# Performance work log

Measured on AMD Instinct MI355X. Metric: run time of the kernel, lower is better.

## Reference

```python
import jax, jax.numpy as jnp
import numpy as np

THRESHOLD = 0.05
TOP_N = 300
NMS_THR = 0.6
POST_TOP_N = 100
MIN_SIZE = 0
N_CLASS = 81
C = N_CLASS - 1
STRIDES = (8, 16, 32, 64, 128)
IMG_H, IMG_W = 800, 1024
B = 16


def _level_hw(s):
    return (-(-IMG_H // s), -(-IMG_W // s))


def setup_inputs() -> dict:
    key = jax.random.key(0)
    inp = {}
    for li, s in enumerate(STRIDES):
        H, W = _level_hw(s)
        key, k1, k2, k3 = jax.random.split(key, 4)
        xs = (jnp.arange(W, dtype=jnp.float32) + 0.5) * s
        ys = (jnp.arange(H, dtype=jnp.float32) + 0.5) * s
        gx, gy = jnp.meshgrid(xs, ys)  # [H, W], row-major h*W+w flatten order
        inp[f"location{li}"] = jnp.stack([gx.reshape(-1), gy.reshape(-1)], -1)
        inp[f"cls{li}"] = jax.random.normal(k1, (B, C, H, W), jnp.float32)
        inp[f"box{li}"] = jax.random.uniform(k2, (B, 4, H, W), jnp.float32) * (4.0 * s)
        inp[f"ctr{li}"] = jax.random.normal(k3, (B, 1, H, W), jnp.float32)
    inp["img_h"] = IMG_H
    inp["img_w"] = IMG_W
    return inp


def _process_level(loc, cls, box, ctr, img_h, img_w):
    b, c, h, w = cls.shape
    cls = jax.nn.sigmoid(cls.transpose(0, 2, 3, 1).reshape(b, h * w, c))
    box = box.transpose(0, 2, 3, 1).reshape(b, h * w, 4)
    ctr = jax.nn.sigmoid(ctr.reshape(b, h * w))
    score = cls * ctr[:, :, None]                 # [B, HW, C]
    masked = jnp.where(cls > THRESHOLD, score, -1.0).reshape(b, -1)
    k = min(TOP_N, masked.shape[1])
    vals, idx = jax.lax.top_k(masked, k)
    if k < TOP_N:
        vals = jnp.pad(vals, ((0, 0), (0, TOP_N - k)), constant_values=-1.0)
        idx = jnp.pad(idx, ((0, 0), (0, TOP_N - k)))
    valid = vals > 0.0                            # candidates only; pads invalid
    pos = idx // c
    label = idx % c + 1
    ssel = jnp.take_along_axis(score.reshape(b, -1), idx, axis=1)  # differentiable gather
    bsel = jnp.take_along_axis(box, pos[..., None], axis=1)        # [B, TOP_N, 4]
    lsel = loc[pos]                                                # [B, TOP_N, 2]
    # decode + clip (BoxList.clip clamps to [0, size-1])
    x1 = jnp.clip(lsel[..., 0] - bsel[..., 0], 0.0, img_w - 1.0)
    y1 = jnp.clip(lsel[..., 1] - bsel[..., 1], 0.0, img_h - 1.0)
    x2 = jnp.clip(lsel[..., 0] + bsel[..., 2], 0.0, img_w - 1.0)
    y2 = jnp.clip(lsel[..., 1] + bsel[..., 3], 0.0, img_h - 1.0)
    det = jnp.stack([x1, y1, x2, y2], -1)
    # remove_small_box: xywh with remove=1
    valid = valid & ((x2 - x1 + 1.0) >= MIN_SIZE) & ((y2 - y1 + 1.0) >= MIN_SIZE)
    scores = jnp.sqrt(jnp.maximum(ssel, 1e-12))
    return det, scores, label, valid


def _pairwise_iou(b):
    area = (b[:, 2] - b[:, 0]) * (b[:, 3] - b[:, 1])
    lt = jnp.maximum(b[:, None, :2], b[None, :, :2])
    rb = jnp.minimum(b[:, None, 2:], b[None, :, 2:])
    wh = jnp.clip(rb - lt, 0.0)
    inter = wh[..., 0] * wh[..., 1]
    union = area[:, None] + area[None, :] - inter
    return inter / jnp.maximum(union, 1e-9)


def _nms_image(boxes, scores, labels, valid, offset):
    # per-class NMS via class-offset trick: boxes of different labels never overlap
    K = boxes.shape[0]
    s = jnp.where(valid, scores, -jnp.inf)
    order = jnp.argsort(-s)
    b = boxes[order]
    v = valid[order]
    lab = labels[order]
    so = s[order]
    iou = _pairwise_iou(b + (lab.astype(b.dtype) * offset)[:, None])
    ar = jnp.arange(K)

    def body(i, keep):
        sup = (iou[i] > NMS_THR) & keep[i] & (ar > i)
        return keep & ~sup

    keep = jax.lax.fori_loop(0, K, body, v)
    s2 = jnp.where(keep, so, -jnp.inf)
    _, idx2 = jax.lax.top_k(s2, POST_TOP_N)   # post_top_n selection
    fvalid = jnp.take(keep, idx2)
    fb = jnp.where(fvalid[:, None], b[idx2], 0.0)
    fs = jnp.where(fvalid, so[idx2], 0.0)
    fl = jnp.where(fvalid, lab[idx2], 0)
    return fb, fs, fl, fvalid


def _forward(locs, clss, boxs, ctrs, img_h, img_w):
    dets, scs, labs, vals = [], [], [], []
    for loc, cl, bx, ct in zip(locs, clss, boxs, ctrs):
        d, s, l, v = _process_level(loc, cl, bx, ct, float(img_h), float(img_w))
        dets.append(d); scs.append(s); labs.append(l); vals.append(v)
    det = jnp.concatenate(dets, 1)   # [B, 5*TOP_N, 4]
    sc = jnp.concatenate(scs, 1)
    lab = jnp.concatenate(labs, 1)
    val = jnp.concatenate(vals, 1)
    offset = float(max(img_h, img_w) + 1)
    fb, fs, fl, fv = jax.vmap(lambda b_, s_, l_, v_: _nms_image(b_, s_, l_, v_, offset))(det, sc, lab, val)
    out5 = jnp.concatenate([fb, fs[..., None]], -1)  # [B, POST_TOP_N, 5]
    return out5, fl, fv


def reference(location0, location1, location2, location3, location4,
              cls0, cls1, cls2, cls3, cls4,
              box0, box1, box2, box3, box4,
              ctr0, ctr1, ctr2, ctr3, ctr4,
              img_h, img_w):
    locs = [location0, location1, location2, location3, location4]
    clss = [cls0, cls1, cls2, cls3, cls4]
    boxs = [box0, box1, box2, box3, box4]
    ctrs = [ctr0, ctr1, ctr2, ctr3, ctr4]
    return _forward(locs, clss, boxs, ctrs, img_h, img_w)
```

## Files before the change

### kernel.cpp

```cpp
#include <hip/hip_runtime.h>
#include <math.h>

#define THREADS 256

constexpr int NLEV  = 5;
constexpr int NB    = 16;
constexpr int NC    = 80;
constexpr int TOPN  = 300;
constexpr int KC    = NLEV * TOPN;
constexpr int KROWS = 1536;
constexpr int WORDS = 24;
constexpr int NTRI  = WORDS * (WORDS + 1) / 2;
constexpr int POSTN = 100;
constexpr int CAP   = 4096;
constexpr int NBINS = 2048;
constexpr int NPAIR = NLEV * NB;

constexpr int HW0 = 12800, HW1 = 3200, HW2 = 800, HW3 = 208, HW4 = 56;
constexpr int CH0 = 63, CH1 = 16, CH2 = 4, CH3 = 2, CH4 = 1;
constexpr int CHUNKS = CH0 + CH1 + CH2 + CH3 + CH4;

constexpr int GPL0 = 4000, GPL1 = 1000, GPL2 = 250, GPL3 = 65, GPL4 = 18;
constexpr int GMXB0 = 0;
constexpr int GMXB1 = GMXB0 + NB * GPL0;
constexpr int GMXB2 = GMXB1 + NB * GPL1;
constexpr int GMXB3 = GMXB2 + NB * GPL2;
constexpr int GMXB4 = GMXB3 + NB * GPL3;
constexpr int GMXN  = GMXB4 + NB * GPL4;

constexpr int BPP = 16;

constexpr int HF_BIG = 1024, HF_SMALL = 1;

constexpr size_t align256(size_t x) { return (x + 255) & ~(size_t)255; }
constexpr size_t OFF_HIST = 0;
constexpr size_t OFF_CNT  = OFF_HIST + (size_t)NPAIR * NBINS * 4;
constexpr size_t OFF_CAND = align256(OFF_CNT + (size_t)NPAIR * 4);
constexpr size_t OFF_CBOX = align256(OFF_CAND + (size_t)NPAIR * CAP * 8);
constexpr size_t OFF_CSC  = align256(OFF_CBOX + (size_t)NB * KC * 4 * 4);
constexpr size_t OFF_CLB  = align256(OFF_CSC  + (size_t)NB * KC * 4);
constexpr size_t OFF_SSC  = align256(OFF_CLB  + (size_t)NB * KC * 4);
constexpr size_t OFF_SLB  = align256(OFF_SSC  + (size_t)NB * KC * 4);
constexpr size_t OFF_SBOX = align256(OFF_SLB  + (size_t)NB * KC * 4);
constexpr size_t OFF_OBOX = align256(OFF_SBOX + (size_t)NB * KC * 4 * 4);
constexpr size_t OFF_M    = align256(OFF_OBOX + (size_t)NB * KC * 4 * 4);
constexpr size_t OFF_GMX  = align256(OFF_M + (size_t)NB * KROWS * WORDS * 8);

struct Cand { float s; int i; };

__device__ __forceinline__ float sigm(float x) { return 1.0f / (1.0f + expf(-x)); }

__device__ __forceinline__ float sigf(float x) {
#if __has_builtin(__builtin_amdgcn_exp2f) && __has_builtin(__builtin_amdgcn_rcpf)
    float e = __builtin_amdgcn_exp2f(__fmul_rn(x, -1.44269504088896340736f));
    return __builtin_amdgcn_rcpf(__fadd_rn(1.0f, e));
#else
    return 1.0f / (1.0f + __expf(-x));
#endif
}

__device__ __forceinline__ unsigned scoreKey(float s) {
    unsigned b = __float_as_uint(s);
    unsigned k = (b < 0x3E800000u) ? 0u : ((b - 0x3E800000u) >> 13);
    return (k > 2047u) ? 2047u : k;
}

__device__ __forceinline__ unsigned long long readlane64(unsigned long long v, int l) {
    unsigned lo = (unsigned)__builtin_amdgcn_readlane((int)(unsigned)(v & 0xffffffffull), l);
    unsigned hi = (unsigned)__builtin_amdgcn_readlane((int)(unsigned)(v >> 32), l);
    return ((unsigned long long)hi << 32) | lo;
}

__device__ void bitonicShared(float* ss, int* si, int N) {
    for (int k = 2; k <= N; k <<= 1) {
        for (int j = k >> 1; j > 0; j >>= 1) {
            __syncthreads();
            for (int i = threadIdx.x; i < N; i += blockDim.x) {
                int ixj = i ^ j;
                if (ixj > i) {
                    float s1 = ss[i], s2 = ss[ixj];
                    int a1 = si[i], a2 = si[ixj];
                    bool bef = (s1 > s2) || (s1 == s2 && a1 < a2);
                    bool up = ((i & k) == 0);
                    if (up ? !bef : bef) { ss[i] = s2; ss[ixj] = s1; si[i] = a2; si[ixj] = a1; }
                }
            }
        }
    }
    __syncthreads();
}

__global__ __launch_bounds__(THREADS) void k_zero(unsigned* __restrict__ zp, int zn) {
    int i = blockIdx.x * THREADS + threadIdx.x;
    if (i < zn) zp[i] = 0;
}

template<int HW, int GPL, int GMXB, int HF>
__device__ __forceinline__ void histChunkV(int chunkLocal, int b,
        const float* __restrict__ cls, const float* __restrict__ ctr,
        unsigned short* __restrict__ gmx, unsigned* __restrict__ h) {
    constexpr int NE = HW * NC;
    const float* cp = cls + (size_t)b * NE;
    const float* tb = ctr + (size_t)b * HW;
    unsigned short* gp = gmx + GMXB + (size_t)b * GPL;
    int w = threadIdx.x >> 6, lane = threadIdx.x & 63;
    int half = lane >> 5, hlane = lane & 31;
    for (int bi = w; bi < 32; bi += 4) {
        int ebase = (chunkLocal * 32 + bi) * 512;
        if (ebase >= NE) break;
        int e = ebase + lane * 8;
        int kmax = 0;
        if (e < NE) {
            int c = e / HW; int hwb = e - c * HW;
            float4 xa = *(const float4*)(cp + e);
            float4 xb = *(const float4*)(cp + e + 4);
            float4 ta = *(const float4*)(tb + hwb);
            float4 tc = *(const float4*)(tb + hwb + 4);
            float xs[8] = {xa.x, xa.y, xa.z, xa.w, xb.x, xb.y, xb.z, xb.w};
            float ts[8] = {ta.x, ta.y, ta.z, ta.w, tc.x, tc.y, tc.z, tc.w};
            #pragma unroll
            for (int q = 0; q < 8; ++q) {
                float scls = sigf(xs[q]);
                float s = __fmul_rn(scls, sigf(ts[q]));
                unsigned key = scoreKey(s);
                if (key >= (unsigned)HF) atomicAdd(&h[key], 1u);
                kmax = max(kmax, (int)key);
            }
        }
        #pragma unroll
        for (int sh = 1; sh < 32; sh <<= 1) kmax = max(kmax, __shfl_xor(kmax, sh, 64));
        int g = (ebase >> 8) + half;
        if (hlane == 0 && g * 256 < NE) gp[g] = (unsigned short)kmax;
    }
}

__global__ __launch_bounds__(THREADS) void k_hist(
        const float* c0, const float* c1, const float* c2, const float* c3, const float* c4,
        const float* t0, const float* t1, const float* t2, const float* t3, const float* t4,
        unsigned short* __restrict__ gmx, unsigned* ghist) {
    __shared__ unsigned h[NBINS];
    for (int k = threadIdx.x; k < NBINS; k += THREADS) h[k] = 0;
    __syncthreads();
    int cx = blockIdx.x, b = blockIdx.y;
    int li;
    if (cx < CH0)                 { histChunkV<HW0,GPL0,GMXB0,HF_BIG>(cx, b, c0, t0, gmx, h); li = 0; }
    else if (cx < CH0+CH1)        { histChunkV<HW1,GPL1,GMXB1,HF_BIG>(cx-CH0, b, c1, t1, gmx, h); li = 1; }
    else if (cx < CH0+CH1+CH2)    { histChunkV<HW2,GPL2,GMXB2,HF_BIG>(cx-CH0-CH1, b, c2, t2, gmx, h); li = 2; }
    else if (cx < CH0+CH1+CH2+CH3){ histChunkV<HW3,GPL3,GMXB3,HF_SMALL>(cx-CH0-CH1-CH2, b, c3, t3, gmx, h); li = 3; }
    else                          { histChunkV<HW4,GPL4,GMXB4,HF_SMALL>(cx-CH0-CH1-CH2-CH3, b, c4, t4, gmx, h); li = 4; }
    __syncthreads();
    unsigned* gp = ghist + (size_t)(li * NB + b) * NBINS;
    for (int k = threadIdx.x; k < NBINS; k += THREADS) {
        unsigned v = h[k];
        if (v) atomicAdd(&gp[k], v);
    }
}

constexpr int LBUF = 1024;
constexpr int GB = 8;

template<int HW>
__device__ __forceinline__ void procList(int b, int pid, unsigned Tv, unsigned n,
        const unsigned short* __restrict__ glist,
        const float* __restrict__ cls, const float* __restrict__ ctr,
        Cand* __restrict__ cd, unsigned* __restrict__ cnt,
        Cand* __restrict__ lbuf, unsigned* __restrict__ lcnt) {
    constexpr int NE = HW * NC;
    const float* cp = cls + (size_t)b * NE;
    const float* tb = ctr + (size_t)b * HW;
    for (unsigned base = 0; base < n; base += GB) {
        float xv[GB], rv[GB];
        int ev[GB];
        bool okv[GB];
        #pragma unroll
        for (int q = 0; q < GB; ++q) {
            unsigned gi = base + q;
            int g = glist[(gi < n) ? gi : (n - 1)];
            int e = g * 256 + (int)threadIdx.x;
            bool ok = (gi < n) && (e < NE);
            e = ok ? e : 0;
            int c = e / HW; int hw = e - c * HW;
            xv[q] = cp[e];
            rv[q] = tb[hw];
            ev[q] = e;
            okv[q] = ok;
        }
        __builtin_amdgcn_sched_barrier(0);
        #pragma unroll
        for (int q = 0; q < GB; ++q) {
            float scls = sigm(xv[q]);
            float s = __fmul_rn(scls, sigm(rv[q]));
            unsigned key = scoreKey(s);
            bool take = okv[q] && (Tv ? (key >= Tv) : (scls > 0.05f));
            if (take) {
                int e = ev[q];
                int c = e / HW; int hw = e - c * HW;
                unsigned slot = atomicAdd(lcnt, 1u);
                if (slot < (unsigned)LBUF) { lbuf[slot].s = s; lbuf[slot].i = hw * NC + c; }
                else {
                    unsigned gs = atomicAdd(&cnt[pid], 1u);
                    if (gs < (unsigned)CAP) { cd[gs].s = s; cd[gs].i = hw * NC + c; }
                }
            }
        }
    }
}

__global__ __launch_bounds__(THREADS) void k_collect(
        const float* c0, const float* c1, const float* c2, const float* c3, const float* c4,
        const float* t0, const float* t1, const float* t2, const float* t3, const float* t4,
        const unsigned* __restrict__ ghist, const unsigned short* __restrict__ gmx,
        Cand* cand, unsigned* cnt) {
    __shared__ unsigned sfx[THREADS];
    __shared__ int tstar;
    __shared__ unsigned shTv;
    __shared__ Cand lbuf[LBUF];
    __shared__ unsigned lcnt, gbase, gcnt;
    __shared__ unsigned short glist[THREADS];
    int tid = (int)threadIdx.x;
    int pid = blockIdx.y;
    int li = pid >> 4, b = pid & 15;
    if (tid == 0) { lcnt = 0; gcnt = 0; tstar = -1; }

    const unsigned* h = ghist + (size_t)pid * NBINS;
    unsigned s = 0;
    #pragma unroll
    for (int k = 0; k < 8; ++k) s += h[tid * 8 + k];
    sfx[tid] = s;
    for (int d = 1; d < THREADS; d <<= 1) {
        __syncthreads();
        unsigned v = (tid + d < THREADS) ? sfx[tid + d] : 0u;
        __syncthreads();
        sfx[tid] += v;
    }
    __syncthreads();
    if (sfx[tid] >= (unsigned)TOPN && (tid == THREADS - 1 || sfx[tid + 1] < (unsigned)TOPN))
        tstar = tid;
    __syncthreads();
    if (tid == 0) {
        unsigned TA = 0;
        int t = tstar;
        if (t >= 0) {
            unsigned acc = (t < THREADS - 1) ? sfx[t + 1] : 0u;
            int lo = t * 8, bin = lo + 7;
            for (; bin >= lo; --bin) { acc += h[bin]; if (acc >= (unsigned)TOPN) break; }
            TA = (unsigned)max(bin, lo);
        }
        shTv = (TA >= 1) ? (TA - 1) : 0u;
    }
    __syncthreads();
    unsigned Tv = shTv;

    int GPL, GMXB;
    switch (li) {
        case 0: GPL = GPL0; GMXB = GMXB0; break;
        case 1: GPL = GPL1; GMXB = GMXB1; break;
        case 2: GPL = GPL2; GMXB = GMXB2; break;
        case 3: GPL = GPL3; GMXB = GMXB3; break;
        default: GPL = GPL4; GMXB = GMXB4; break;
    }
    const unsigned short* gp = gmx + GMXB + (size_t)b * GPL;
    int per = (GPL + BPP - 1) / BPP;
    int lo = (int)blockIdx.x * per;
    int hi = min(GPL, lo + per);
    {
        int g = lo + tid;
        bool ok = (g < hi);
        if (ok && Tv) ok = ((unsigned)gp[g] + 1u >= Tv);
        unsigned long long m = __ballot(ok);
        int nW = __popcll(m);
        if (nW) {
            unsigned wb = 0;
            if ((tid & 63) == 0) wb = atomicAdd(&gcnt, (unsigned)nW);
            wb = (unsigned)__builtin_amdgcn_readfirstlane((int)wb);
            if (ok) glist[wb + (unsigned)__popcll(m & ((1ull << (tid & 63)) - 1ull))] = (unsigned short)g;
        }
    }
    __syncthreads();
    unsigned n = gcnt;
    Cand* cd = cand + (size_t)pid * CAP;
    if (n) {
        switch (li) {
            case 0: procList<HW0>(b, pid, Tv, n, glist, c0, t0, cd, cnt, lbuf, &lcnt); break;
            case 1: procList<HW1>(b, pid, Tv, n, glist, c1, t1, cd, cnt, lbuf, &lcnt); break;
            case 2: procList<HW2>(b, pid, Tv, n, glist, c2, t2, cd, cnt, lbuf, &lcnt); break;
            case 3: procList<HW3>(b, pid, Tv, n, glist, c3, t3, cd, cnt, lbuf, &lcnt); break;
            default: procList<HW4>(b, pid, Tv, n, glist, c4, t4, cd, cnt, lbuf, &lcnt); break;
        }
    }
    __syncthreads();
    unsigned nl = lcnt; if (nl > (unsigned)LBUF) nl = LBUF;
    if (tid == 0) gbase = nl ? atomicAdd(&cnt[pid], nl) : 0u;
    __syncthreads();
    for (unsigned i = tid; i < nl; i += THREADS) {
        unsigned sl = gbase + i;
        if (sl < (unsigned)CAP) cd[sl] = lbuf[i];
    }
}

__global__ __launch_bounds__(THREADS) void k_select(
        const Cand* __restrict__ candAll, const unsigned* __restrict__ cntAll,
        const float* l0, const float* l1, const float* l2, const float* l3, const float* l4,
        const float* b0, const float* b1, const float* b2, const float* b3, const float* b4,
        float* __restrict__ cbox, float* __restrict__ csc, int* __restrict__ clb) {
    __shared__ float ss[CAP];
    __shared__ int si[CAP];
    int pid = blockIdx.x;
    int li = pid / NB, b = pid - li * NB;
    int n = (int)min(cntAll[pid], (unsigned)CAP);
    const Cand* cd = candAll + (size_t)pid * CAP;
    int N = 2; while (N < n) N <<= 1;
    for (int k = threadIdx.x; k < N; k += THREADS) {
        if (k < n) { ss[k] = cd[k].s; si[k] = cd[k].i; }
        else       { ss[k] = -INFINITY; si[k] = 0x40000000 + k; }
    }
    __syncthreads();
    bitonicShared(ss, si, N);

    const float* locp; const float* boxp; int HW;
    switch (li) {
        case 0: locp = l0; boxp = b0; HW = HW0; break;
        case 1: locp = l1; boxp = b1; HW = HW1; break;
        case 2: locp = l2; boxp = b2; HW = HW2; break;
        case 3: locp = l3; boxp = b3; HW = HW3; break;
        default: locp = l4; boxp = b4; HW = HW4; break;
    }
    for (int j = threadIdx.x; j < TOPN; j += THREADS) {
        int cidx = b * KC + li * TOPN + j;
        bool ok = (j < n);
        float s = ok ? ss[j] : -INFINITY;
        ok = ok && (s > 0.0f);
        if (ok) {
            int idx = si[j];
            int hw = idx / NC, c = idx - hw * NC;
            float lx = locp[hw * 2 + 0], ly = locp[hw * 2 + 1];
            const float* bp = boxp + (size_t)b * 4 * HW + hw;
            float bl = bp[0], bt = bp[HW], br = bp[2 * HW], bb = bp[3 * HW];
            float x1 = fminf(fmaxf(__fsub_rn(lx, bl), 0.0f), 1023.0f);
            float y1 = fminf(fmaxf(__fsub_rn(ly, bt), 0.0f),  799.0f);
            float x2 = fminf(fmaxf(__fadd_rn(lx, br), 0.0f), 1023.0f);
            float y2 = fminf(fmaxf(__fadd_rn(ly, bb), 0.0f),  799.0f);
            cbox[cidx * 4 + 0] = x1; cbox[cidx * 4 + 1] = y1;
            cbox[cidx * 4 + 2] = x2; cbox[cidx * 4 + 3] = y2;
            csc[cidx] = sqrtf(fmaxf(s, 1e-12f));
            clb[cidx] = c + 1;
        } else {
            cbox[cidx * 4 + 0] = 0.0f; cbox[cidx * 4 + 1] = 0.0f;
            cbox[cidx * 4 + 2] = 0.0f; cbox[cidx * 4 + 3] = 0.0f;
            csc[cidx] = -INFINITY;
            clb[cidx] = 0;
        }
    }
}

__global__ __launch_bounds__(THREADS) void k_merge(
        const float* __restrict__ csc, const int* __restrict__ clb, const float* __restrict__ cbox,
        float* __restrict__ ssc, int* __restrict__ slb, float* __restrict__ sbox,
        float* __restrict__ obox) {
    int li = blockIdx.x, b = blockIdx.y;
    __shared__ float ss[KC];
    for (int k = threadIdx.x; k < KC; k += THREADS) ss[k] = csc[b * KC + k];
    __syncthreads();
    for (int j = threadIdx.x; j < TOPN; j += THREADS) {
        int k = li * TOPN + j;
        float s = ss[k];
        int rank = j;
        #pragma unroll
        for (int l = 0; l < NLEV; ++l) {
            if (l == li) continue;
            const float* seg = ss + l * TOPN;
            int lo = 0, hi = TOPN;
            if (l < li) {
                while (lo < hi) { int m = (lo + hi) >> 1; if (seg[m] >= s) lo = m + 1; else hi = m; }
            } else {
                while (lo < hi) { int m = (lo + hi) >> 1; if (seg[m] >  s) lo = m + 1; else hi = m; }
            }
            rank += lo;
        }
        int src = b * KC + k, dst = b * KC + rank;
        int lab = clb[src];
        ssc[dst] = s; slb[dst] = lab;
        float off = __fmul_rn((float)lab, 1025.0f);
        float4 v = *(const float4*)&cbox[(size_t)src * 4];
        *(float4*)&sbox[(size_t)dst * 4] = v;
        float4 o;
        o.x = __fadd_rn(v.x, off); o.y = __fadd_rn(v.y, off);
        o.z = __fadd_rn(v.z, off); o.w = __fadd_rn(v.w, off);
        *(float4*)&obox[(size_t)dst * 4] = o;
    }
}

__global__ __launch_bounds__(64) void k_iou(const float* __restrict__ obox,
                                            unsigned long long* __restrict__ MT) {
    int t = blockIdx.x, b = blockIdx.y;
    int tile = 0, rem = t;
    while (rem >= WORDS - tile) { rem -= WORDS - tile; ++tile; }
    int w = tile + rem;
    int lane = threadIdx.x;
    __shared__ float4 sj[64];
    __shared__ float aj[64];
    const float4* op = (const float4*)obox + (size_t)b * KC;
    int j0 = w * 64;
    int jl = j0 + lane;
    float4 vj = op[(jl < KC) ? jl : (KC - 1)];
    sj[lane] = vj;
    aj[lane] = __fmul_rn(__fsub_rn(vj.z, vj.x), __fsub_rn(vj.w, vj.y));
    int i = tile * 64 + lane;
    float4 bi = op[(i < KC) ? i : (KC - 1)];
    float ai = __fmul_rn(__fsub_rn(bi.z, bi.x), __fsub_rn(bi.w, bi.y));
    __syncthreads();
    unsigned long long bits = 0;
    int jmax = min(64, KC - j0);
    for (int jj = 0; jj < jmax; ++jj) {
        float4 bj = sj[jj];
        float xx1 = fmaxf(bi.x, bj.x), yy1 = fmaxf(bi.y, bj.y);
        float xx2 = fminf(bi.z, bj.z), yy2 = fminf(bi.w, bj.w);
        float ww = fmaxf(__fsub_rn(xx2, xx1), 0.0f);
        float hh = fmaxf(__fsub_rn(yy2, yy1), 0.0f);
        float inter = __fmul_rn(ww, hh);
        float uni = __fsub_rn(__fadd_rn(ai, aj[jj]), inter);
        float iou = __fdiv_rn(inter, fmaxf(uni, 1e-9f));
        bool kp = ((j0 + jj) > i) && (iou > 0.6f);
        bits |= kp ? (1ull << jj) : 0ull;
    }
    if (i >= KC) bits = 0;
    MT[((size_t)b * WORDS + w) * KROWS + i] = bits;
}

__global__ __launch_bounds__(64) void k_nms(
        const unsigned long long* __restrict__ MT, const float* __restrict__ ssc,
        const int* __restrict__ slb, const float* __restrict__ sbox, float* __restrict__ out) {
    int b = blockIdx.x, lane = threadIdx.x;
    for (int k = lane; k < POSTN * 5; k += 64) out[(size_t)b * POSTN * 5 + k] = 0.0f;
    for (int k = lane; k < POSTN; k += 64) {
        out[(size_t)NB * POSTN * 5 + b * POSTN + k] = 0.0f;
        out[(size_t)NB * POSTN * 5 + NB * POSTN + b * POSTN + k] = 0.0f;
    }
    const float* sp = ssc + b * KC;
    unsigned long long validV = 0;
    for (int c = 0; c < WORDS; ++c) {
        int i = c * 64 + lane;
        bool f = (i < KC) && (sp[i] > 0.0f);
        unsigned long long m = __ballot(f);
        validV = (lane == c) ? m : validV;
    }
    unsigned long long mybit = 1ull << lane;
    unsigned long long keptV = 0;
    const unsigned long long* Mb = MT + (size_t)b * WORDS * KROWS;

    unsigned long long pv[WORDS];
    pv[0] = Mb[lane];

    int keptTotal = 0;
    for (int t = 0; t < WORDS; ++t) {
        int tn = (t + 1 < WORDS) ? (t + 1) : t;
        const unsigned long long* cp = Mb + (size_t)tn * KROWS + lane;
        unsigned long long nv[WORDS];
        #pragma unroll
        for (int c = 0; c < WORDS; ++c) {
            int cc = (c <= tn) ? c : 0;
            nv[c] = cp[(size_t)cc * 64];
        }
        __builtin_amdgcn_sched_barrier(0);

        unsigned long long D = pv[t];
        unsigned long long acc = 0;
        #pragma unroll
        for (int c = 0; c < WORDS; ++c) {
            if (c < t) {
                unsigned long long kc = readlane64(keptV, c);
                if (kc & mybit) acc |= pv[c];
            }
        }
        #pragma unroll
        for (int s = 1; s < 64; s <<= 1) acc |= __shfl_xor(acc, s, 64);

        unsigned long long validT = readlane64(validV, t);
        unsigned long long rem = acc;
        unsigned long long sup = __ballot(D != 0ull) & validT;
        unsigned long long todoS = sup;
        while (todoS) {
            int r = __builtin_ctzll(todoS);
            todoS &= todoS - 1;
            if (!((rem >> r) & 1ull)) {
                unsigned long long Dr = readlane64(D, r);
                rem |= Dr;
                todoS &= ~Dr;
            }
        }
        unsigned long long kept = validT & ~rem;
        keptV = (lane == t) ? kept : keptV;

        keptTotal += (int)__popcll(kept);
        if (keptTotal >= POSTN) break;

        #pragma unroll
        for (int c = 0; c < WORDS; ++c) pv[c] = nv[c];
    }

    int base = 0;
    for (int c = 0; c < WORDS && base < POSTN; ++c) {
        unsigned long long kw = readlane64(keptV, c);
        bool f = (kw & mybit) != 0ull;
        int rank = base + __popcll(kw & (mybit - 1ull));
        if (f && rank < POSTN) {
            int i = c * 64 + lane;
            int src = b * KC + i;
            float* o5 = out + ((size_t)b * POSTN + rank) * 5;
            o5[0] = sbox[src * 4 + 0]; o5[1] = sbox[src * 4 + 1];
            o5[2] = sbox[src * 4 + 2]; o5[3] = sbox[src * 4 + 3];
            o5[4] = ssc[src];
            out[(size_t)NB * POSTN * 5 + b * POSTN + rank] = (float)slb[src];
            out[(size_t)NB * POSTN * 5 + NB * POSTN + b * POSTN + rank] = 1.0f;
        }
        base += __popcll(kw);
    }
}

extern "C" void kernel_launch(void* const* d_in, const int* in_sizes, int n_in,
                              void* d_out, int out_size, void* d_ws, size_t ws_size,
                              hipStream_t stream) {
    const float *loc[5], *cls[5], *box[5], *ctr[5];
    for (int l = 0; l < 5; ++l) {
        loc[l] = (const float*)d_in[l * 4 + 0];
        cls[l] = (const float*)d_in[l * 4 + 1];
        box[l] = (const float*)d_in[l * 4 + 2];
        ctr[l] = (const float*)d_in[l * 4 + 3];
    }
    char* ws = (char*)d_ws;
    unsigned* hist = (unsigned*)(ws + OFF_HIST);
    unsigned* cnt  = (unsigned*)(ws + OFF_CNT);
    Cand* cand     = (Cand*)(ws + OFF_CAND);
    float* cbox    = (float*)(ws + OFF_CBOX);
    float* csc     = (float*)(ws + OFF_CSC);
    int*   clb     = (int*)(ws + OFF_CLB);
    float* ssc     = (float*)(ws + OFF_SSC);
    int*   slb     = (int*)(ws + OFF_SLB);
    float* sbox    = (float*)(ws + OFF_SBOX);
    float* obox    = (float*)(ws + OFF_OBOX);
    unsigned long long* MT = (unsigned long long*)(ws + OFF_M);
    unsigned short* gmx = (unsigned short*)(ws + OFF_GMX);
    float* out = (float*)d_out;

    int zn = (int)(OFF_CAND / 4);
    k_zero<<<(zn + THREADS - 1) / THREADS, THREADS, 0, stream>>>((unsigned*)ws, zn);
    k_hist<<<dim3(CHUNKS, NB), THREADS, 0, stream>>>(
        cls[0], cls[1], cls[2], cls[3], cls[4],
        ctr[0], ctr[1], ctr[2], ctr[3], ctr[4], gmx, hist);
    k_collect<<<dim3(BPP, NPAIR), THREADS, 0, stream>>>(
        cls[0], cls[1], cls[2], cls[3], cls[4],
        ctr[0], ctr[1], ctr[2], ctr[3], ctr[4], hist, gmx, cand, cnt);
    k_select<<<NPAIR, THREADS, 0, stream>>>(
        cand, cnt,
        loc[0], loc[1], loc[2], loc[3], loc[4],
        box[0], box[1], box[2], box[3], box[4],
        cbox, csc, clb);
    k_merge<<<dim3(NLEV, NB), THREADS, 0, stream>>>(csc, clb, cbox, ssc, slb, sbox, obox);
    k_iou<<<dim3(NTRI, NB), 64, 0, stream>>>(obox, MT);
    k_nms<<<NB, 64, 0, stream>>>(MT, ssc, slb, sbox, out);
}
```

Baseline: 240.2 us.

## Fuse merge, IoU mask and NMS into one per-image 1024-thread kernel

```diff
diff --git a/kernel.cpp b/kernel.cpp
--- a/kernel.cpp
+++ b/kernel.cpp
@@ -39,11 +39,7 @@
 constexpr size_t OFF_CBOX = align256(OFF_CAND + (size_t)NPAIR * CAP * 8);
 constexpr size_t OFF_CSC  = align256(OFF_CBOX + (size_t)NB * KC * 4 * 4);
 constexpr size_t OFF_CLB  = align256(OFF_CSC  + (size_t)NB * KC * 4);
-constexpr size_t OFF_SSC  = align256(OFF_CLB  + (size_t)NB * KC * 4);
-constexpr size_t OFF_SLB  = align256(OFF_SSC  + (size_t)NB * KC * 4);
-constexpr size_t OFF_SBOX = align256(OFF_SLB  + (size_t)NB * KC * 4);
-constexpr size_t OFF_OBOX = align256(OFF_SBOX + (size_t)NB * KC * 4 * 4);
-constexpr size_t OFF_M    = align256(OFF_OBOX + (size_t)NB * KC * 4 * 4);
+constexpr size_t OFF_M    = align256(OFF_CLB  + (size_t)NB * KC * 4);
 constexpr size_t OFF_GMX  = align256(OFF_M + (size_t)NB * KROWS * WORDS * 8);
 
 struct Cand { float s; int i; };
@@ -353,22 +349,29 @@
     }
 }
 
-__global__ __launch_bounds__(THREADS) void k_merge(
-        const float* __restrict__ csc, const int* __restrict__ clb, const float* __restrict__ cbox,
-        float* __restrict__ ssc, int* __restrict__ slb, float* __restrict__ sbox,
-        float* __restrict__ obox) {
-    int li = blockIdx.x, b = blockIdx.y;
-    __shared__ float ss[KC];
-    for (int k = threadIdx.x; k < KC; k += THREADS) ss[k] = csc[b * KC + k];
-    __syncthreads();
-    for (int j = threadIdx.x; j < TOPN; j += THREADS) {
-        int k = li * TOPN + j;
-        float s = ss[k];
+__global__ __launch_bounds__(1024) void k_final(
+        const float* __restrict__ csc, const int* __restrict__ clb,
+        const float* __restrict__ cbox,
+        unsigned long long* __restrict__ MT, float* __restrict__ out) {
+    __shared__ float  sin_l[KC];
+    __shared__ float  ssc_l[KC];
+    __shared__ int    slb_l[KC];
+    __shared__ float4 sbox_l[KC];
+    __shared__ float4 obox_l[KC];
+    __shared__ float  area_l[KC];
+    int b = blockIdx.x;
+    int tid = (int)threadIdx.x;
+
+    for (int k = tid; k < KC; k += 1024) sin_l[k] = csc[b * KC + k];
+    __syncthreads();
+    for (int k = tid; k < KC; k += 1024) {
+        int li = k / TOPN, j = k - li * TOPN;
+        float s = sin_l[k];
         int rank = j;
         #pragma unroll
         for (int l = 0; l < NLEV; ++l) {
             if (l == li) continue;
-            const float* seg = ss + l * TOPN;
+            const float* seg = sin_l + l * TOPN;
             int lo = 0, hi = TOPN;
             if (l < li) {
                 while (lo < hi) { int m = (lo + hi) >> 1; if (seg[m] >= s) lo = m + 1; else hi = m; }
@@ -377,143 +380,133 @@
             }
             rank += lo;
         }
-        int src = b * KC + k, dst = b * KC + rank;
+        int src = b * KC + k;
         int lab = clb[src];
-        ssc[dst] = s; slb[dst] = lab;
+        ssc_l[rank] = s;
+        slb_l[rank] = lab;
         float off = __fmul_rn((float)lab, 1025.0f);
         float4 v = *(const float4*)&cbox[(size_t)src * 4];
-        *(float4*)&sbox[(size_t)dst * 4] = v;
+        sbox_l[rank] = v;
         float4 o;
         o.x = __fadd_rn(v.x, off); o.y = __fadd_rn(v.y, off);
         o.z = __fadd_rn(v.z, off); o.w = __fadd_rn(v.w, off);
-        *(float4*)&obox[(size_t)dst * 4] = o;
-    }
-}
-
-__global__ __launch_bounds__(64) void k_iou(const float* __restrict__ obox,
-                                            unsigned long long* __restrict__ MT) {
-    int t = blockIdx.x, b = blockIdx.y;
-    int tile = 0, rem = t;
-    while (rem >= WORDS - tile) { rem -= WORDS - tile; ++tile; }
-    int w = tile + rem;
-    int lane = threadIdx.x;
-    __shared__ float4 sj[64];
-    __shared__ float aj[64];
-    const float4* op = (const float4*)obox + (size_t)b * KC;
-    int j0 = w * 64;
-    int jl = j0 + lane;
-    float4 vj = op[(jl < KC) ? jl : (KC - 1)];
-    sj[lane] = vj;
-    aj[lane] = __fmul_rn(__fsub_rn(vj.z, vj.x), __fsub_rn(vj.w, vj.y));
-    int i = tile * 64 + lane;
-    float4 bi = op[(i < KC) ? i : (KC - 1)];
-    float ai = __fmul_rn(__fsub_rn(bi.z, bi.x), __fsub_rn(bi.w, bi.y));
-    __syncthreads();
-    unsigned long long bits = 0;
-    int jmax = min(64, KC - j0);
-    for (int jj = 0; jj < jmax; ++jj) {
-        float4 bj = sj[jj];
-        float xx1 = fmaxf(bi.x, bj.x), yy1 = fmaxf(bi.y, bj.y);
-        float xx2 = fminf(bi.z, bj.z), yy2 = fminf(bi.w, bj.w);
-        float ww = fmaxf(__fsub_rn(xx2, xx1), 0.0f);
-        float hh = fmaxf(__fsub_rn(yy2, yy1), 0.0f);
-        float inter = __fmul_rn(ww, hh);
-        float uni = __fsub_rn(__fadd_rn(ai, aj[jj]), inter);
-        float iou = __fdiv_rn(inter, fmaxf(uni, 1e-9f));
-        bool kp = ((j0 + jj) > i) && (iou > 0.6f);
-        bits |= kp ? (1ull << jj) : 0ull;
-    }
-    if (i >= KC) bits = 0;
-    MT[((size_t)b * WORDS + w) * KROWS + i] = bits;
-}
-
-__global__ __launch_bounds__(64) void k_nms(
-        const unsigned long long* __restrict__ MT, const float* __restrict__ ssc,
-        const int* __restrict__ slb, const float* __restrict__ sbox, float* __restrict__ out) {
-    int b = blockIdx.x, lane = threadIdx.x;
-    for (int k = lane; k < POSTN * 5; k += 64) out[(size_t)b * POSTN * 5 + k] = 0.0f;
-    for (int k = lane; k < POSTN; k += 64) {
-        out[(size_t)NB * POSTN * 5 + b * POSTN + k] = 0.0f;
-        out[(size_t)NB * POSTN * 5 + NB * POSTN + b * POSTN + k] = 0.0f;
-    }
-    const float* sp = ssc + b * KC;
-    unsigned long long validV = 0;
-    for (int c = 0; c < WORDS; ++c) {
-        int i = c * 64 + lane;
-        bool f = (i < KC) && (sp[i] > 0.0f);
-        unsigned long long m = __ballot(f);
-        validV = (lane == c) ? m : validV;
-    }
-    unsigned long long mybit = 1ull << lane;
-    unsigned long long keptV = 0;
-    const unsigned long long* Mb = MT + (size_t)b * WORDS * KROWS;
-
-    unsigned long long pv[WORDS];
-    pv[0] = Mb[lane];
-
-    int keptTotal = 0;
-    for (int t = 0; t < WORDS; ++t) {
-        int tn = (t + 1 < WORDS) ? (t + 1) : t;
-        const unsigned long long* cp = Mb + (size_t)tn * KROWS + lane;
-        unsigned long long nv[WORDS];
-        #pragma unroll
+        obox_l[rank] = o;
+        area_l[rank] = __fmul_rn(__fsub_rn(o.z, o.x), __fsub_rn(o.w, o.y));
+    }
+    __syncthreads();
+
+    int wid = tid >> 6, lane = tid & 63;
+    for (int t = wid; t < NTRI; t += 16) {
+        int tile = 0, rem = t;
+        while (rem >= WORDS - tile) { rem -= WORDS - tile; ++tile; }
+        int w = tile + rem;
+        int j0 = w * 64;
+        int i = tile * 64 + lane;
+        int ic = (i < KC) ? i : (KC - 1);
+        float4 bi = obox_l[ic];
+        float ai = area_l[ic];
+        unsigned long long bits = 0;
+        int jmax = min(64, KC - j0);
+        for (int jj = 0; jj < jmax; ++jj) {
+            float4 bj = obox_l[j0 + jj];
+            float xx1 = fmaxf(bi.x, bj.x), yy1 = fmaxf(bi.y, bj.y);
+            float xx2 = fminf(bi.z, bj.z), yy2 = fminf(bi.w, bj.w);
+            float ww = fmaxf(__fsub_rn(xx2, xx1), 0.0f);
+            float hh = fmaxf(__fsub_rn(yy2, yy1), 0.0f);
+            float inter = __fmul_rn(ww, hh);
+            float uni = __fsub_rn(__fadd_rn(ai, area_l[j0 + jj]), inter);
+            float iou = __fdiv_rn(inter, fmaxf(uni, 1e-9f));
+            bool kp = ((j0 + jj) > i) && (iou > 0.6f);
+            bits |= kp ? (1ull << jj) : 0ull;
+        }
+        if (i >= KC) bits = 0;
+        MT[((size_t)b * WORDS + w) * KROWS + i] = bits;
+    }
+    __syncthreads();
+
+    if (tid < 64) {
+        for (int k = lane; k < POSTN * 5; k += 64) out[(size_t)b * POSTN * 5 + k] = 0.0f;
+        for (int k = lane; k < POSTN; k += 64) {
+            out[(size_t)NB * POSTN * 5 + b * POSTN + k] = 0.0f;
+            out[(size_t)NB * POSTN * 5 + NB * POSTN + b * POSTN + k] = 0.0f;
+        }
+        unsigned long long validV = 0;
         for (int c = 0; c < WORDS; ++c) {
-            int cc = (c <= tn) ? c : 0;
-            nv[c] = cp[(size_t)cc * 64];
-        }
-        __builtin_amdgcn_sched_barrier(0);
-
-        unsigned long long D = pv[t];
-        unsigned long long acc = 0;
-        #pragma unroll
-        for (int c = 0; c < WORDS; ++c) {
-            if (c < t) {
-                unsigned long long kc = readlane64(keptV, c);
-                if (kc & mybit) acc |= pv[c];
-            }
-        }
-        #pragma unroll
-        for (int s = 1; s < 64; s <<= 1) acc |= __shfl_xor(acc, s, 64);
-
-        unsigned long long validT = readlane64(validV, t);
-        unsigned long long rem = acc;
-        unsigned long long sup = __ballot(D != 0ull) & validT;
-        unsigned long long todoS = sup;
-        while (todoS) {
-            int r = __builtin_ctzll(todoS);
-            todoS &= todoS - 1;
-            if (!((rem >> r) & 1ull)) {
-                unsigned long long Dr = readlane64(D, r);
-                rem |= Dr;
-                todoS &= ~Dr;
-            }
-        }
-        unsigned long long kept = validT & ~rem;
-        keptV = (lane == t) ? kept : keptV;
-
-        keptTotal += (int)__popcll(kept);
-        if (keptTotal >= POSTN) break;
-
-        #pragma unroll
-        for (int c = 0; c < WORDS; ++c) pv[c] = nv[c];
-    }
-
-    int base = 0;
-    for (int c = 0; c < WORDS && base < POSTN; ++c) {
-        unsigned long long kw = readlane64(keptV, c);
-        bool f = (kw & mybit) != 0ull;
-        int rank = base + __popcll(kw & (mybit - 1ull));
-        if (f && rank < POSTN) {
             int i = c * 64 + lane;
-            int src = b * KC + i;
-            float* o5 = out + ((size_t)b * POSTN + rank) * 5;
-            o5[0] = sbox[src * 4 + 0]; o5[1] = sbox[src * 4 + 1];
-            o5[2] = sbox[src * 4 + 2]; o5[3] = sbox[src * 4 + 3];
-            o5[4] = ssc[src];
-            out[(size_t)NB * POSTN * 5 + b * POSTN + rank] = (float)slb[src];
-            out[(size_t)NB * POSTN * 5 + NB * POSTN + b * POSTN + rank] = 1.0f;
-        }
-        base += __popcll(kw);
+            bool f = (i < KC) && (ssc_l[i] > 0.0f);
+            unsigned long long m = __ballot(f);
+            validV = (lane == c) ? m : validV;
+        }
+        unsigned long long mybit = 1ull << lane;
+        unsigned long long keptV = 0;
+        const unsigned long long* Mb = MT + (size_t)b * WORDS * KROWS;
+
+        unsigned long long pv[WORDS];
+        pv[0] = Mb[lane];
+
+        int keptTotal = 0;
+        for (int t = 0; t < WORDS; ++t) {
+            int tn = (t + 1 < WORDS) ? (t + 1) : t;
+            const unsigned long long* cp = Mb + (size_t)tn * KROWS + lane;
+            unsigned long long nv[WORDS];
+            #pragma unroll
+            for (int c = 0; c < WORDS; ++c) {
+                int cc = (c <= tn) ? c : 0;
+                nv[c] = cp[(size_t)cc * 64];
+            }
+            __builtin_amdgcn_sched_barrier(0);
+
+            unsigned long long D = pv[t];
+            unsigned long long acc = 0;
+            #pragma unroll
+            for (int c = 0; c < WORDS; ++c) {
+                if (c < t) {
+                    unsigned long long kc = readlane64(keptV, c);
+                    if (kc & mybit) acc |= pv[c];
+                }
+            }
+            #pragma unroll
+            for (int s = 1; s < 64; s <<= 1) acc |= __shfl_xor(acc, s, 64);
+
+            unsigned long long validT = readlane64(validV, t);
+            unsigned long long rem = acc;
+            unsigned long long sup = __ballot(D != 0ull) & validT;
+            unsigned long long todoS = sup;
+            while (todoS) {
+                int r = __builtin_ctzll(todoS);
+                todoS &= todoS - 1;
+                if (!((rem >> r) & 1ull)) {
+                    unsigned long long Dr = readlane64(D, r);
+                    rem |= Dr;
+                    todoS &= ~Dr;
+                }
+            }
+            unsigned long long kept = validT & ~rem;
+            keptV = (lane == t) ? kept : keptV;
+
+            keptTotal += (int)__popcll(kept);
+            if (keptTotal >= POSTN) break;
+
+            #pragma unroll
+            for (int c = 0; c < WORDS; ++c) pv[c] = nv[c];
+        }
+
+        int base = 0;
+        for (int c = 0; c < WORDS && base < POSTN; ++c) {
+            unsigned long long kw = readlane64(keptV, c);
+            bool f = (kw & mybit) != 0ull;
+            int rank = base + __popcll(kw & (mybit - 1ull));
+            if (f && rank < POSTN) {
+                int i = c * 64 + lane;
+                float4 v = sbox_l[i];
+                float* o5 = out + ((size_t)b * POSTN + rank) * 5;
+                o5[0] = v.x; o5[1] = v.y; o5[2] = v.z; o5[3] = v.w;
+                o5[4] = ssc_l[i];
+                out[(size_t)NB * POSTN * 5 + b * POSTN + rank] = (float)slb_l[i];
+                out[(size_t)NB * POSTN * 5 + NB * POSTN + b * POSTN + rank] = 1.0f;
+            }
+            base += __popcll(kw);
+        }
     }
 }
 
@@ -534,10 +527,6 @@
     float* cbox    = (float*)(ws + OFF_CBOX);
     float* csc     = (float*)(ws + OFF_CSC);
     int*   clb     = (int*)(ws + OFF_CLB);
-    float* ssc     = (float*)(ws + OFF_SSC);
-    int*   slb     = (int*)(ws + OFF_SLB);
-    float* sbox    = (float*)(ws + OFF_SBOX);
-    float* obox    = (float*)(ws + OFF_OBOX);
     unsigned long long* MT = (unsigned long long*)(ws + OFF_M);
     unsigned short* gmx = (unsigned short*)(ws + OFF_GMX);
     float* out = (float*)d_out;
@@ -555,7 +544,5 @@
         loc[0], loc[1], loc[2], loc[3], loc[4],
         box[0], box[1], box[2], box[3], box[4],
         cbox, csc, clb);
-    k_merge<<<dim3(NLEV, NB), THREADS, 0, stream>>>(csc, clb, cbox, ssc, slb, sbox, obox);
-    k_iou<<<dim3(NTRI, NB), 64, 0, stream>>>(obox, MT);
-    k_nms<<<NB, 64, 0, stream>>>(MT, ssc, slb, sbox, out);
-}
+    k_final<<<NB, 1024, 0, stream>>>(csc, clb, cbox, MT, out);
+}
```

After: 470.7 us. 1.96x slower.
